# Optimization experiments

Measured on AMD Instinct MI355X. Metric: run time of the kernel, lower is better.

## Reference

```python
import jax, jax.numpy as jnp
import numpy as np

NUM_HEADS = 16


def setup_inputs() -> dict:
    key = jax.random.key(0)
    ks = jax.random.split(key, 7)
    B, S, H = 2, 2048, 1024
    x = jax.random.normal(ks[0], (B, S, H), dtype=jnp.float32)
    y = jax.random.normal(ks[1], (B, S, H), dtype=jnp.float32)
    bias = jnp.zeros((B, 1, 1, S), dtype=jnp.float32)  # additive attention bias (padding mask)
    w_scale = 0.02
    wq = jax.random.normal(ks[2], (H, H), dtype=jnp.float32) * w_scale
    wk = jax.random.normal(ks[3], (H, H), dtype=jnp.float32) * w_scale
    wv = jax.random.normal(ks[4], (H, H), dtype=jnp.float32) * w_scale
    wo = jax.random.normal(ks[5], (H, H), dtype=jnp.float32) * w_scale
    return {"x": x, "y": y, "bias": bias, "wq": wq, "wk": wk, "wv": wv, "wo": wo}


def reference(x, y, bias, wq, wk, wv, wo):
    B, S, H = x.shape
    nh = NUM_HEADS
    dh = H // nh
    # QKV projections, split heads: [B, S, H] -> [B, nh, S, dh]
    q = jnp.einsum("bsh,hd->bsd", x, wq).reshape(B, S, nh, dh).transpose(0, 2, 1, 3)
    k = jnp.einsum("bsh,hd->bsd", y, wk).reshape(B, S, nh, dh).transpose(0, 2, 1, 3)
    v = jnp.einsum("bsh,hd->bsd", y, wv).reshape(B, S, nh, dh).transpose(0, 2, 1, 3)
    # Scale queries (tensor2tensor convention: q *= size_per_head ** -0.5)
    q = q * (dh ** -0.5)
    logits = jnp.einsum("bhqd,bhkd->bhqk", q, k) + bias  # [B, nh, S, S]
    weights = jax.nn.softmax(logits, axis=-1)
    # (attention_dropout = 0.0 -> identity)
    ctx = jnp.einsum("bhqk,bhkd->bhqd", weights, v)  # [B, nh, S, dh]
    ctx = ctx.transpose(0, 2, 1, 3).reshape(B, S, H)  # combine heads
    return jnp.einsum("bsh,hd->bsd", ctx, wo)
```

## Files before the change

kernel.cpp:

```cpp
#include <hip/hip_runtime.h>

using u16 = unsigned short;
using u32 = unsigned int;

typedef __bf16 bf16x8 __attribute__((ext_vector_type(8)));
typedef __bf16 bf16x4 __attribute__((ext_vector_type(4)));
typedef float f32x4 __attribute__((ext_vector_type(4)));
typedef u16 u16x4 __attribute__((ext_vector_type(4)));

#define GLD_LDS16(gp, lp)                                                                 \
  __builtin_amdgcn_global_load_lds((const __attribute__((address_space(1))) void*)(gp),   \
                                   (__attribute__((address_space(3))) void*)(lp), 16, 0, 0)

__device__ __forceinline__ u16 f2b(float f) {
  union { float f; u32 u; } v; v.f = f;
  return (u16)((v.u + 0x7fffu + ((v.u >> 16) & 1u)) >> 16);
}

__device__ __forceinline__ void pl32swap(u32& a, u32& b) {
  asm("v_permlane32_swap_b32 %0, %1" : "+v"(a), "+v"(b));
}
__device__ __forceinline__ void pl16swap(u32& a, u32& b) {
  asm("v_permlane16_swap_b32 %0, %1" : "+v"(a), "+v"(b));
}
__device__ __forceinline__ u32 cvtpk(float lo, float hi) {
  u32 d; asm("v_cvt_pk_bf16_f32 %0, %1, %2" : "=v"(d) : "v"(lo), "v"(hi));
  return d;
}
__device__ __forceinline__ float red4_max(float x) {
  union { float f; u32 u; } a, b;
  a.f = x;
  asm("v_mov_b32 %0, %1" : "=v"(b.u) : "v"(a.u));
  asm("v_permlane32_swap_b32 %0, %1" : "+v"(a.u), "+v"(b.u));
  union { float f; u32 u; } m, c;
  m.f = fmaxf(a.f, b.f);
  asm("v_mov_b32 %0, %1" : "=v"(c.u) : "v"(m.u));
  asm("v_permlane16_swap_b32 %0, %1" : "+v"(m.u), "+v"(c.u));
  return fmaxf(m.f, c.f);
}
#define EXP2(x) __builtin_amdgcn_exp2f(x)

__global__ __launch_bounds__(256) void prep(
    const float* __restrict__ w0, const float* __restrict__ w1,
    const float* __restrict__ w2, const float* __restrict__ w3,
    u16* __restrict__ o0, u16* __restrict__ o1,
    u16* __restrict__ o2, u16* __restrict__ o3,
    const float* __restrict__ x, const float* __restrict__ y,
    u16* __restrict__ xb, u16* __restrict__ yb,
    const float* __restrict__ bias, float* __restrict__ bs) {
  __shared__ float tile[64][65];
  int z = blockIdx.z;
  if (z < 4) {
    const float* src; u16* dst;
    switch (z) {
      case 0: src = w0; dst = o0; break;
      case 1: src = w1; dst = o1; break;
      case 2: src = w2; dst = o2; break;
      default: src = w3; dst = o3; break;
    }
    int bx = blockIdx.x * 64, by = blockIdx.y * 64;
    int tx = threadIdx.x & 63, ty = threadIdx.x >> 6;
    for (int r = ty; r < 64; r += 4)
      tile[r][tx] = src[(size_t)(by + r) * 1024 + bx + tx];
    __syncthreads();
    for (int r = ty; r < 64; r += 4)
      dst[(size_t)(bx + r) * 1024 + by + tx] = f2b(tile[tx][r]);
  } else if (z < 6) {
    const float* src = (z == 4) ? x : y;
    u16* dst = (z == 4) ? xb : yb;
    size_t base = ((size_t)(blockIdx.y * 16 + blockIdx.x) * 256 + threadIdx.x) * 8;
    const size_t step = (size_t)256 * 256 * 8, total = (size_t)4096 * 1024;
    for (size_t i = base; i < total; i += step) {
      float4 f0 = *(const float4*)(src + i);
      float4 f1 = *(const float4*)(src + i + 4);
      bf16x8 v;
      v[0] = (__bf16)f0.x; v[1] = (__bf16)f0.y; v[2] = (__bf16)f0.z; v[3] = (__bf16)f0.w;
      v[4] = (__bf16)f1.x; v[5] = (__bf16)f1.y; v[6] = (__bf16)f1.z; v[7] = (__bf16)f1.w;
      *(bf16x8*)(dst + i) = v;
    }
  } else {
    if (blockIdx.x == 0 && blockIdx.y == 0)
      for (int i = threadIdx.x; i < 4096; i += 256)
        bs[i] = bias[i] * 1.44269504088896f;
  }
}

#define BM 128
#define BK 64

__global__ __launch_bounds__(256) void gemm_qkv(
    const u16* __restrict__ xb, const u16* __restrict__ yb, const u16* __restrict__ wT,
    u16* __restrict__ Qb, u16* __restrict__ Kb, u16* __restrict__ Vb) {
  __shared__ __align__(16) u16 As[BM * BK];
  __shared__ __align__(16) u16 Bs[64 * BK];
  const int K = 1024;
  int region = blockIdx.y >> 4;
  const u16* A = (region == 0) ? xb : yb;
  const u16* BT = wT + (size_t)region * 1024 * 1024;
  float scale = (region == 0) ? 0.125f * 1.44269504088896f : 1.0f;
  int tid = threadIdx.x;
  int wave = tid >> 6, lane = tid & 63;
  int r = lane & 15, kg = lane >> 4;
  int lhi = lane >> 3, llo = lane & 7;
  int bm = blockIdx.x * BM, bn = (blockIdx.y & 15) * 64;
  int wr = (wave >> 1) * 64, wc = (wave & 1) * 32;
  f32x4 acc[4][2] = {};

  const u16* Ag = A + (size_t)(bm + wave * 32 + lhi) * K + llo * 8;
  const u16* Bg = BT + (size_t)(bn + wave * 16 + lhi) * K + llo * 8;
  u16* Asb = As + wave * 32 * BK;
  u16* Bsb = Bs + wave * 16 * BK;

  for (int k0 = 0; k0 < K; k0 += BK) {
#pragma unroll
    for (int c = 0; c < 4; ++c)
      GLD_LDS16(Ag + (size_t)c * 8 * K + k0, Asb + c * 8 * BK);
#pragma unroll
    for (int c = 0; c < 2; ++c)
      GLD_LDS16(Bg + (size_t)c * 8 * K + k0, Bsb + c * 8 * BK);
    __syncthreads();
#pragma unroll
    for (int kk = 0; kk < 2; ++kk) {
      bf16x8 af[4], bfv[2];
#pragma unroll
      for (int m = 0; m < 4; ++m)
        af[m] = *(const bf16x8*)&As[(wr + m * 16 + r) * BK + kk * 32 + kg * 8];
#pragma unroll
      for (int n = 0; n < 2; ++n)
        bfv[n] = *(const bf16x8*)&Bs[(wc + n * 16 + r) * BK + kk * 32 + kg * 8];
#pragma unroll
      for (int m = 0; m < 4; ++m)
#pragma unroll
        for (int n = 0; n < 2; ++n)
          acc[m][n] = __builtin_amdgcn_mfma_f32_16x16x32_bf16(af[m], bfv[n], acc[m][n], 0, 0, 0);
    }
    __syncthreads();
  }

  if (region == 2) {
#pragma unroll
    for (int m = 0; m < 4; ++m)
#pragma unroll
      for (int n = 0; n < 2; ++n) {
        int row0 = bm + wr + m * 16 + kg * 4;
        int col = bn + wc + n * 16 + r;
        int bb = row0 >> 11, s = row0 & 2047;
        int hh = col >> 6, dd = col & 63;
        u16x4 pk;
#pragma unroll
        for (int i = 0; i < 4; ++i) pk[i] = f2b(acc[m][n][i]);
        *(u16x4*)&Vb[((size_t)(bb * 16 + hh) * 64 + dd) * 2048 + s] = pk;
      }
  } else {
    u16* dst = (region == 0) ? Qb : Kb;
#pragma unroll
    for (int m = 0; m < 4; ++m)
#pragma unroll
      for (int n = 0; n < 2; ++n)
#pragma unroll
        for (int i = 0; i < 4; ++i) {
          int row = bm + wr + m * 16 + kg * 4 + i;
          int col = bn + wc + n * 16 + r;
          dst[(size_t)row * 1024 + col] = f2b(acc[m][n][i] * scale);
        }
  }
}

__global__ __launch_bounds__(256) void gemm_wo(
    const u16* __restrict__ A, const u16* __restrict__ BT, float* __restrict__ Cp,
    float scale) {
  __shared__ __align__(16) u16 As[64 * BK];
  __shared__ __align__(16) u16 Bs[64 * BK];
  const int K = 1024, N = 1024;
  int tid = threadIdx.x;
  int wave = tid >> 6, lane = tid & 63;
  int r = lane & 15, kg = lane >> 4;
  int lhi = lane >> 3, llo = lane & 7;
  int bm = blockIdx.x * 64, bn = blockIdx.y * 64;
  int wr = (wave >> 1) * 32, wc = (wave & 1) * 32;
  f32x4 acc[2][2] = {};

  const u16* Ag = A + (size_t)(bm + wave * 16 + lhi) * K + llo * 8;
  const u16* Bg = BT + (size_t)(bn + wave * 16 + lhi) * K + llo * 8;
  u16* Asb = As + wave * 16 * BK;
  u16* Bsb = Bs + wave * 16 * BK;

  for (int k0 = 0; k0 < K; k0 += BK) {
#pragma unroll
    for (int c = 0; c < 2; ++c) {
      GLD_LDS16(Ag + (size_t)c * 8 * K + k0, Asb + c * 8 * BK);
      GLD_LDS16(Bg + (size_t)c * 8 * K + k0, Bsb + c * 8 * BK);
    }
    __syncthreads();
#pragma unroll
    for (int kk = 0; kk < 2; ++kk) {
      bf16x8 af[2], bfv[2];
#pragma unroll
      for (int m = 0; m < 2; ++m)
        af[m] = *(const bf16x8*)&As[(wr + m * 16 + r) * BK + kk * 32 + kg * 8];
#pragma unroll
      for (int n = 0; n < 2; ++n)
        bfv[n] = *(const bf16x8*)&Bs[(wc + n * 16 + r) * BK + kk * 32 + kg * 8];
#pragma unroll
      for (int m = 0; m < 2; ++m)
#pragma unroll
        for (int n = 0; n < 2; ++n)
          acc[m][n] = __builtin_amdgcn_mfma_f32_16x16x32_bf16(af[m], bfv[n], acc[m][n], 0, 0, 0);
    }
    __syncthreads();
  }

#pragma unroll
  for (int m = 0; m < 2; ++m)
#pragma unroll
    for (int n = 0; n < 2; ++n)
#pragma unroll
      for (int i = 0; i < 4; ++i) {
        int row = bm + wr + m * 16 + kg * 4 + i;
        int col = bn + wc + n * 16 + r;
        Cp[(size_t)row * N + col] = acc[m][n][i] * scale;
      }
}

__global__ __launch_bounds__(512) void flash_attn(
    const u16* __restrict__ Q, const u16* __restrict__ Km, const u16* __restrict__ VtG,
    const float* __restrict__ biasS, u16* __restrict__ ctx) {
  const int S = 2048, H = 1024;
  __shared__ __align__(16) u16 Ks[2][64 * 64];
  __shared__ __align__(16) u16 Vs[2][64 * 64];
  int tid = threadIdx.x;
  int wave = tid >> 6, lane = tid & 63;
  int r = lane & 15, kg = lane >> 4;
  int h = blockIdx.x, b = blockIdx.y, qt = blockIdx.z;

  const u16* Qb = Q + (size_t)(b * S + qt * 128 + wave * 16 + r) * H + h * 64 + kg * 8;
  bf16x8 qa[2];
  qa[0] = *(const bf16x8*)(Qb);
  qa[1] = *(const bf16x8*)(Qb + 32);

  bf16x8 onesv;
#pragma unroll
  for (int j = 0; j < 8; ++j) onesv[j] = (__bf16)1.0f;

  int lhi = lane >> 3, llo = lane & 7;
  int ksch = llo ^ lhi;
  const u16* KgB = Km + (size_t)b * S * H + h * 64;
  const u16* VgB = VtG + ((size_t)(b * 16 + h) * 64) * 2048;
  const float* biasB = biasS + (size_t)b * S;

  float m_i = -1e30f;
  f32x4 acc[4] = {};
  f32x4 acc_l = {};

  auto issueKV = [&](int kv0, int bi) {
    GLD_LDS16(KgB + (size_t)(kv0 + wave * 8 + lhi) * H + ksch * 8,
              &Ks[bi][wave * 8 * 64]);
    GLD_LDS16(VgB + (size_t)(wave * 8 + lhi) * 2048 + kv0 + ksch * 8,
              &Vs[bi][wave * 8 * 64]);
  };
  auto issueB = [&](int kv0, f32x4* bv) {
#pragma unroll
    for (int n = 0; n < 4; ++n)
      bv[n] = *(const f32x4*)(biasB + kv0 + n * 16 + (kg << 2));
  };

  auto compute = [&](const u16* KsB, const u16* VsB, const f32x4* bv) {
    f32x4 sv[4];
#pragma unroll
    for (int n = 0; n < 4; ++n) sv[n] = bv[n];
    __builtin_amdgcn_s_setprio(1);
#pragma unroll
    for (int kk = 0; kk < 2; ++kk)
#pragma unroll
      for (int n = 0; n < 4; ++n) {
        bf16x8 kb = *(const bf16x8*)&KsB[(n * 16 + r) * 64 +
                                         ((((kk << 2) + kg) ^ (r & 7)) << 3)];
        sv[n] = __builtin_amdgcn_mfma_f32_16x16x32_bf16(kb, qa[kk], sv[n], 0, 0, 0);
      }
    __builtin_amdgcn_s_setprio(0);

    float m0 = fmaxf(fmaxf(sv[0][0], sv[0][1]), fmaxf(sv[0][2], sv[0][3]));
    float m1 = fmaxf(fmaxf(sv[1][0], sv[1][1]), fmaxf(sv[1][2], sv[1][3]));
    float m2 = fmaxf(fmaxf(sv[2][0], sv[2][1]), fmaxf(sv[2][2], sv[2][3]));
    float m3 = fmaxf(fmaxf(sv[3][0], sv[3][1]), fmaxf(sv[3][2], sv[3][3]));
    float mx = red4_max(fmaxf(fmaxf(m0, m1), fmaxf(m2, m3)));
    float sc = 1.f;
    if (mx > m_i + 8.f) { sc = EXP2(m_i - mx); m_i = mx; }
    if (__any(sc != 1.f)) {
#pragma unroll
      for (int i = 0; i < 4; ++i) {
        float sci = __shfl(sc, (lane & 48) | ((kg << 2) + i));
#pragma unroll
        for (int n = 0; n < 4; ++n) acc[n][i] *= sci;
        acc_l[i] *= sci;
      }
    }
    float e[4][4];
#pragma unroll
    for (int n = 0; n < 4; ++n)
#pragma unroll
      for (int i = 0; i < 4; ++i)
        e[n][i] = EXP2(sv[n][i] - m_i);

    u32 w[4][2];
#pragma unroll
    for (int n = 0; n < 4; ++n) {
      w[n][0] = cvtpk(e[n][0], e[n][1]);
      w[n][1] = cvtpk(e[n][2], e[n][3]);
    }

    __builtin_amdgcn_s_setprio(1);
#pragma unroll
    for (int kk = 0; kk < 2; ++kk) {
      u32 a0 = w[2 * kk][0], a1 = w[2 * kk][1];
      u32 b0 = w[2 * kk + 1][0], b1 = w[2 * kk + 1][1];
      pl32swap(a0, b0); pl32swap(a1, b1);
      pl16swap(a0, b0); pl16swap(a1, b1);
      union { u32 u[4]; bf16x8 v; } pa;
      pa.u[0] = a0; pa.u[1] = a1; pa.u[2] = b0; pa.u[3] = b1;
#pragma unroll
      for (int n = 0; n < 4; ++n) {
        bf16x8 vb = *(const bf16x8*)&VsB[(n * 16 + r) * 64 +
                                         ((((kk << 2) + kg) ^ (r & 7)) << 3)];
        acc[n] = __builtin_amdgcn_mfma_f32_16x16x32_bf16(pa.v, vb, acc[n], 0, 0, 0);
      }
      acc_l = __builtin_amdgcn_mfma_f32_16x16x32_bf16(pa.v, onesv, acc_l, 0, 0, 0);
    }
    __builtin_amdgcn_s_setprio(0);
  };

  f32x4 bp[4], bn2[4];

  issueKV(0, 0); issueB(0, bp);
  __syncthreads();

  for (int t2 = 0; t2 < 16; ++t2) {
    int kv1 = (t2 * 2 + 1) * 64;
    int kv2 = ((t2 * 2 + 2) & 31) * 64;
    issueKV(kv1, 1); issueB(kv1, bn2);
    compute(Ks[0], Vs[0], bp);
    __syncthreads();
    issueKV(kv2, 0); issueB(kv2, bp);
    compute(Ks[1], Vs[1], bn2);
    __syncthreads();
  }

#pragma unroll
  for (int i = 0; i < 4; ++i) {
    float inv = 1.0f / acc_l[i];
    size_t row = (size_t)(b * S + qt * 128 + wave * 16 + (kg << 2) + i);
#pragma unroll
    for (int n = 0; n < 4; ++n)
      ctx[row * H + h * 64 + n * 16 + r] = f2b(acc[n][i] * inv);
  }
}

extern "C" void kernel_launch(void* const* d_in, const int* in_sizes, int n_in,
                              void* d_out, int out_size, void* d_ws, size_t ws_size,
                              hipStream_t stream) {
  const float* x    = (const float*)d_in[0];
  const float* y    = (const float*)d_in[1];
  const float* bias = (const float*)d_in[2];
  const float* wq   = (const float*)d_in[3];
  const float* wk   = (const float*)d_in[4];
  const float* wv   = (const float*)d_in[5];
  const float* wo   = (const float*)d_in[6];
  float* out = (float*)d_out;

  u16* ws = (u16*)d_ws;
  const size_t WELEM = 1024 * 1024;
  const size_t MELEM = (size_t)4096 * 1024;
  u16* wqT = ws;
  u16* wkT = wqT + WELEM;
  u16* wvT = wkT + WELEM;
  u16* woT = wvT + WELEM;
  u16* Qb  = woT + WELEM;
  u16* Kb  = Qb + MELEM;
  u16* Vb  = Kb + MELEM;
  u16* xb  = Vb + MELEM;
  u16* yb  = xb + MELEM;
  float* bs = (float*)(yb + MELEM);
  u16* Cb  = Qb;

  dim3 blk(256);
  prep<<<dim3(16, 16, 7), blk, 0, stream>>>(wq, wk, wv, wo, wqT, wkT, wvT, woT,
                                            x, y, xb, yb, bias, bs);
  gemm_qkv<<<dim3(32, 48), blk, 0, stream>>>(xb, yb, wqT, Qb, Kb, Vb);
  flash_attn<<<dim3(16, 2, 16), dim3(512), 0, stream>>>(Qb, Kb, Vb, bs, Cb);
  gemm_wo<<<dim3(64, 16), blk, 0, stream>>>(Cb, woT, out, 1.0f);
}
```

Before: 134.3 us.

## Software-pipeline flash attention: overlap next-tile QK with current softmax-PV

```diff
diff --git a/kernel.cpp b/kernel.cpp
--- a/kernel.cpp
+++ b/kernel.cpp
@@ -226,8 +226,8 @@
     const u16* __restrict__ Q, const u16* __restrict__ Km, const u16* __restrict__ VtG,
     const float* __restrict__ biasS, u16* __restrict__ ctx) {
   const int S = 2048, H = 1024;
-  __shared__ __align__(16) u16 Ks[2][64 * 64];
-  __shared__ __align__(16) u16 Vs[2][64 * 64];
+  __shared__ __align__(16) u16 Ks[3][64 * 64];
+  __shared__ __align__(16) u16 Vs[3][64 * 64];
   int tid = threadIdx.x;
   int wave = tid >> 6, lane = tid & 63;
   int r = lane & 15, kg = lane >> 4;
@@ -252,20 +252,19 @@
   f32x4 acc[4] = {};
   f32x4 acc_l = {};
 
-  auto issueKV = [&](int kv0, int bi) {
+  auto stage = [&](int kv0, int bi) {
     GLD_LDS16(KgB + (size_t)(kv0 + wave * 8 + lhi) * H + ksch * 8,
               &Ks[bi][wave * 8 * 64]);
     GLD_LDS16(VgB + (size_t)(wave * 8 + lhi) * 2048 + kv0 + ksch * 8,
               &Vs[bi][wave * 8 * 64]);
   };
-  auto issueB = [&](int kv0, f32x4* bv) {
+  auto loadB = [&](int kv0, f32x4* bv) {
 #pragma unroll
     for (int n = 0; n < 4; ++n)
       bv[n] = *(const f32x4*)(biasB + kv0 + n * 16 + (kg << 2));
   };
 
-  auto compute = [&](const u16* KsB, const u16* VsB, const f32x4* bv) {
-    f32x4 sv[4];
+  auto qk = [&](const u16* KsB, const f32x4* bv, f32x4* sv) {
 #pragma unroll
     for (int n = 0; n < 4; ++n) sv[n] = bv[n];
     __builtin_amdgcn_s_setprio(1);
@@ -278,7 +277,9 @@
         sv[n] = __builtin_amdgcn_mfma_f32_16x16x32_bf16(kb, qa[kk], sv[n], 0, 0, 0);
       }
     __builtin_amdgcn_s_setprio(0);
-
+  };
+
+  auto smpv = [&](const f32x4* sv, const u16* VsB) {
     float m0 = fmaxf(fmaxf(sv[0][0], sv[0][1]), fmaxf(sv[0][2], sv[0][3]));
     float m1 = fmaxf(fmaxf(sv[1][0], sv[1][1]), fmaxf(sv[1][2], sv[1][3]));
     float m2 = fmaxf(fmaxf(sv[2][0], sv[2][1]), fmaxf(sv[2][2], sv[2][3]));
@@ -329,21 +330,30 @@
     __builtin_amdgcn_s_setprio(0);
   };
 
-  f32x4 bp[4], bn2[4];
-
-  issueKV(0, 0); issueB(0, bp);
+  f32x4 svA[4], svB[4];
+  f32x4 bvA[4], bvB[4];
+
+  stage(0, 0); loadB(0, bvA);
   __syncthreads();
-
-  for (int t2 = 0; t2 < 16; ++t2) {
-    int kv1 = (t2 * 2 + 1) * 64;
-    int kv2 = ((t2 * 2 + 2) & 31) * 64;
-    issueKV(kv1, 1); issueB(kv1, bn2);
-    compute(Ks[0], Vs[0], bp);
-    __syncthreads();
-    issueKV(kv2, 0); issueB(kv2, bp);
-    compute(Ks[1], Vs[1], bn2);
-    __syncthreads();
-  }
+  stage(64, 1); loadB(64, bvB);
+  qk(Ks[0], bvA, svA);
+  __syncthreads();
+
+  auto body = [&](int t, f32x4* svCur, f32x4* svNext, f32x4* bvNext, f32x4* bvLoad) {
+    int tp = (t + 2) & 31;
+    stage(tp * 64, (t + 2) % 3);
+    loadB(tp * 64, bvLoad);
+    qk(Ks[(t + 1) % 3], bvNext, svNext);
+    smpv(svCur, Vs[t % 3]);
+    __syncthreads();
+  };
+
+  for (int t2 = 0; t2 < 15; ++t2) {
+    body(2 * t2,     svA, svB, bvB, bvA);
+    body(2 * t2 + 1, svB, svA, bvA, bvB);
+  }
+  body(30, svA, svB, bvB, bvA);
+  smpv(svB, Vs[31 % 3]);
 
 #pragma unroll
   for (int i = 0; i < 4; ++i) {
```

Result: slower. 156.4 us (+16.4%).
